# Kernel tuning notes

Hardware: AMD Instinct MI355X
Metric: run time of the kernel (lower is better)

Reference implementation:

```python
import jax, jax.numpy as jnp
import numpy as np

CHN = 64
C8 = CHN // 8          # 8
ANG_IN = 5
ANG_OUT = 5
BU, V, H, W = 8, ANG_IN, 64, 64


def setup_inputs() -> dict:
    key = jax.random.key(0)
    ks = jax.random.split(key, 7)
    s = 0.05
    buffer = jax.random.normal(ks[0], (BU, CHN, V, H, W), jnp.float32)
    # 1x1x1 Conv3d weights stored as [out_ch, in_ch]
    Wq = jax.random.normal(ks[1], (C8, CHN), jnp.float32) * s
    Wk = jax.random.normal(ks[2], (C8, CHN), jnp.float32) * s
    Wv = jax.random.normal(ks[3], (C8 * ANG_OUT, CHN), jnp.float32) * s
    Wc = jax.random.normal(ks[4], (C8 * ANG_OUT, CHN), jnp.float32) * s
    # out block: Conv3d(40->64, k=(1,1,7), pad (0,0,3)); Conv3d(64->64, k=(7,1,1), pad (3,0,0))
    W1 = jax.random.normal(ks[5], (CHN, C8 * ANG_IN, 1, 1, 7), jnp.float32) * s
    W2 = jax.random.normal(ks[6], (CHN, CHN, 7, 1, 1), jnp.float32) * s
    return {"buffer": buffer, "Wq": Wq, "Wk": Wk, "Wv": Wv, "Wc": Wc, "W1": W1, "W2": W2}


def _pointwise(Wo, x):
    # 1x1x1 Conv3d == channel GEMM
    return jnp.einsum('oc,bcvhw->bovhw', Wo, x)


def reference(buffer, Wq, Wk, Wv, Wc, W1, W2):
    bu, c, v, h, w = buffer.shape
    q = _pointwise(Wq, buffer)      # [bu, c8, v, h, w]
    k = _pointwise(Wk, buffer)      # [bu, c8, v, h, w]
    val = _pointwise(Wv, buffer)    # [bu, c8*ar_out, v, h, w]

    def flat(x):  # 'bu c v h w -> bu c h (v w)'
        return x.transpose(0, 1, 3, 2, 4).reshape(bu, x.shape[1], h, v * w)

    qf, kf, vf = flat(q), flat(k), flat(val)
    attn = jax.nn.softmax(jnp.einsum('bchm,bchn->bhmn', qf, kf), axis=-1)  # [bu,h,vw,vw]
    out = jnp.einsum('bhmn,bchn->bchm', attn, vf)                          # [bu,c8*ar_out,h,vw]
    out = out.reshape(bu, -1, h, v, w).transpose(0, 1, 3, 2, 4)            # [bu,c8*ar_out,v,h,w]

    out = out + _pointwise(Wc, buffer)
    # 'bu (c ar_out) v h w -> bu (c v) ar_out h w'
    c8 = out.shape[1] // ANG_OUT
    out = out.reshape(bu, c8, ANG_OUT, v, h, w).transpose(0, 1, 3, 2, 4, 5)
    out = out.reshape(bu, c8 * v, ANG_OUT, h, w)

    dn = ('NCDHW', 'OIDHW', 'NCDHW')
    out = jax.nn.relu(jax.lax.conv_general_dilated(
        out, W1, (1, 1, 1), [(0, 0), (0, 0), (3, 3)], dimension_numbers=dn))
    out = jax.nn.relu(jax.lax.conv_general_dilated(
        out, W2, (1, 1, 1), [(3, 3), (0, 0), (0, 0)], dimension_numbers=dn))
    return out  # [bu, chn, ar_out, h, w]
```

## Files before the change

kernel.cpp:

```cpp
#include <hip/hip_runtime.h>
#include <math.h>


typedef __attribute__((ext_vector_type(8))) short bf16x8;
typedef __attribute__((ext_vector_type(4))) short bf16x4;
typedef __attribute__((ext_vector_type(4))) float fp32x4;
typedef __attribute__((ext_vector_type(8))) unsigned short u16x8;

#define OFF_WP      0
#define OFF_Z       29696
#define OFF_W1P_US  12288
#define OFF_W2P_US  30720
#define OFF_QFH_US  13166592
#define OFF_KFH_US  14477312
#define OFF_VTH_US  15788032

__device__ inline unsigned short f2b(float f) {
    unsigned u = __builtin_bit_cast(unsigned, f);
    u = (u + 0x7fffu + ((u >> 16) & 1u)) >> 16;
    return (unsigned short)u;
}

#if __has_builtin(__builtin_amdgcn_mfma_f32_16x16x16bf16_1k)
#define MFMA16(a, b, c) __builtin_amdgcn_mfma_f32_16x16x16bf16_1k(a, b, c, 0, 0, 0)
#else
static __device__ inline fp32x4 mfma16_asm(bf16x4 a, bf16x4 b, fp32x4 c) {
    asm("v_mfma_f32_16x16x16_bf16 %0, %1, %2, %0" : "+v"(c) : "v"(a), "v"(b));
    return c;
}
#define MFMA16(a, b, c) mfma16_asm(a, b, c)
#endif

__global__ void prep_weights(const float* __restrict__ Wq, const float* __restrict__ Wk,
                             const float* __restrict__ Wv, const float* __restrict__ Wc,
                             const float* __restrict__ W1, const float* __restrict__ W2,
                             float* __restrict__ ws) {
    int e = blockIdx.x * 256 + threadIdx.x;
    unsigned short* us = (unsigned short*)ws;
    if (e < 6144) {
        int og = e / 1536, r = e % 1536;
        int c = r / 24, l = r % 24;
        int o = og * 24 + l;
        float v;
        if (o < 8)       v = Wq[o * 64 + c];
        else if (o < 16) v = Wk[(o - 8) * 64 + c];
        else if (o < 56) v = Wv[(o - 16) * 64 + c];
        else             v = Wc[(o - 56) * 64 + c];
        ws[OFF_WP + e] = v;
    } else if (e < 6144 + 18432) {
        int t = e - 6144;
        int j = t & 7, lane = (t >> 3) & 63, ks = (t >> 9) % 9, wid = t / 4608;
        int oc = wid * 16 + (lane & 15);
        int k = ks * 32 + (lane >> 4) * 8 + j;
        float v = 0.f;
        if (k < 280) { int kw = k / 40, ic = k % 40; v = W1[oc * 280 + ic * 7 + kw]; }
        us[OFF_W1P_US + t] = f2b(v);
    } else if (e < 6144 + 18432 + 28672) {
        int t = e - 6144 - 18432;
        int j = t & 7, lane = (t >> 3) & 63, kk = (t >> 9) & 1, kd = (t >> 10) % 7, wid = t / 7168;
        int oc = wid * 16 + (lane & 15);
        int ic = kk * 32 + (lane >> 4) * 8 + j;
        us[OFF_W2P_US + t] = f2b(W2[oc * 448 + ic * 7 + kd]);
    }
}

__global__ __launch_bounds__(256) void proj_kernel(const float* __restrict__ buf,
                                                   float* __restrict__ ws) {
    __shared__ alignas(16) float xs[64 * 64];
    int b = blockIdx.x;
    int h = b & 63;
    int v = (b >> 6) % 5;
    int bu = b / 320;
    int tid = threadIdx.x, wid = tid >> 6, w = tid & 63;

    const float* xbase = buf + ((bu * 64) * 5 + v) * 4096 + h * 64;
    for (int e = tid; e < 1024; e += 256) {
        int c = e >> 4, wq = e & 15;
        *(float4*)&xs[c * 64 + wq * 4] = *(const float4*)&xbase[c * 20480 + wq * 4];
    }
    __syncthreads();

    int og = __builtin_amdgcn_readfirstlane(wid);
    const float* wp = ws + OFF_WP + og * 1536;

    float acc[24];
    #pragma unroll
    for (int l = 0; l < 24; l++) acc[l] = 0.f;
    for (int c = 0; c < 64; c++) {
        float x = xs[c * 64 + w];
        const float* wr = wp + c * 24;
        #pragma unroll
        for (int l = 0; l < 24; l++) acc[l] += wr[l] * x;
    }

    int site = bu * 64 + h;
    int n = v * 64 + w;
    unsigned short* base = (unsigned short*)ws;
    unsigned short* qfh = base + OFF_QFH_US;
    unsigned short* kfh = base + OFF_KFH_US;
    unsigned short* vth = base + OFF_VTH_US;
    float* z = ws + OFF_Z;

    if (og == 0) {
        u16x8 qv, kv;
        #pragma unroll
        for (int l = 0; l < 8; l++) { qv[l] = f2b(acc[l]); kv[l] = f2b(acc[8 + l]); }
        *(u16x8*)&qfh[(site * 320 + n) * 8] = qv;
        *(u16x8*)&kfh[(site * 320 + n) * 8] = kv;
        #pragma unroll
        for (int l = 16; l < 24; l++) vth[(site * 48 + (l - 16)) * 320 + n] = f2b(acc[l]);
    } else if (og == 1) {
        #pragma unroll
        for (int l = 0; l < 24; l++) vth[(site * 48 + 8 + l) * 320 + n] = f2b(acc[l]);
    } else if (og == 2) {
        #pragma unroll
        for (int l = 0; l < 8; l++) vth[(site * 48 + 32 + l) * 320 + n] = f2b(acc[l]);
        #pragma unroll
        for (int l = 8; l < 24; l++) {
            int j2 = l - 8;
            int c8 = j2 / 5, ar = j2 % 5;
            z[((bu * 40 + c8 * 5 + v) * 5 + ar) * 4096 + h * 64 + w] = acc[l];
        }
    } else {
        #pragma unroll
        for (int l = 0; l < 24; l++) {
            int j2 = 16 + l;
            int c8 = j2 / 5, ar = j2 % 5;
            z[((bu * 40 + c8 * 5 + v) * 5 + ar) * 4096 + h * 64 + w] = acc[l];
        }
        #pragma unroll
        for (int j = 40; j < 48; j++)
            vth[(site * 48 + j) * 320 + n] = (j == 40) ? (unsigned short)0x3F80 : (unsigned short)0;
    }
}

__global__ __launch_bounds__(256, 2) void attn_kernel(float* __restrict__ ws) {
    __shared__ alignas(16) short vt[48 * 328];

    int bid = blockIdx.x;
    int chunk = bid >> 9;
    int site = bid & 511;
    int bu = site >> 6, h = site & 63;
    int tid = threadIdx.x;
    int wid = tid >> 6, lane = tid & 63;
    int col = lane & 15, quad = lane >> 4;

    const unsigned short* base = (const unsigned short*)ws;
    const unsigned short* qfh = base + OFF_QFH_US + site * 320 * 8;
    const unsigned short* kfh = base + OFF_KFH_US + site * 320 * 8;
    const unsigned short* vsrc = base + OFF_VTH_US + site * 48 * 320;
    float* z = ws + OFF_Z;

    for (int e = tid; e < 48 * 40; e += 256) {
        int row = e / 40, c8o = e % 40;
        *(u16x8*)&vt[row * 328 + c8o * 8] = *(const u16x8*)&vsrc[row * 320 + c8o * 8];
    }
    __syncthreads();

    int off0[4], off1[4], off2[4];
    #pragma unroll
    for (int r = 0; r < 4; r++) {
        int j0 = quad * 4 + r, j1 = j0 + 16, j2 = j0 + 32;
        off0[r] = ((j0 / 5) * 25 + j0 % 5) * 4096;
        off1[r] = ((j1 / 5) * 25 + j1 % 5) * 4096;
        off2[r] = ((j2 / 5) * 25 + j2 % 5) * 4096;
    }

    int mt = chunk * 4 + wid;
    int m0 = mt * 16;

    bf16x8 qa = (bf16x8)0;
    if (quad == 0) qa = *(const bf16x8*)&qfh[(m0 + col) * 8];

    fp32x4 acc0 = {0.f, 0.f, 0.f, 0.f}, acc1 = acc0, acc2 = acc0;

    for (int cc = 0; cc < 4; cc++) {
        fp32x4 sT[5];
        #pragma unroll
        for (int u = 0; u < 5; u++) {
            int nt = cc * 5 + u;
            bf16x8 kb = (bf16x8)0;
            if (quad == 0) kb = *(const bf16x8*)&kfh[(nt * 16 + col) * 8];
            sT[u] = __builtin_amdgcn_mfma_f32_16x16x32_bf16(
                kb, qa, (fp32x4){0.f, 0.f, 0.f, 0.f}, 0, 0, 0);
        }
        #pragma unroll
        for (int u = 0; u < 5; u++) {
            int nt = cc * 5 + u;
            bf16x4 pa;
            #pragma unroll
            for (int r = 0; r < 4; r++) pa[r] = (short)f2b(__expf(sT[u][r]));
            const short* vb = &vt[nt * 16 + quad * 4];
            acc0 = MFMA16(*(const bf16x4*)&vb[(col) * 328],      pa, acc0);
            acc1 = MFMA16(*(const bf16x4*)&vb[(16 + col) * 328], pa, acc1);
            acc2 = MFMA16(*(const bf16x4*)&vb[(32 + col) * 328], pa, acc2);
        }
    }

    float L = __shfl(acc2[0], 32 + col, 64);
    float inv = 1.f / L;

    int v_idx = m0 >> 6, w0 = m0 & 63;
    float* zb = z + (bu * 200 + v_idx * 5) * 4096 + h * 64 + w0 + col;
    #pragma unroll
    for (int r = 0; r < 4; r++) {
        zb[off0[r]] += acc0[r] * inv;
        zb[off1[r]] += acc1[r] * inv;
        if (quad < 2) zb[off2[r]] += acc2[r] * inv;
    }
}

__global__ __launch_bounds__(256) void conv12_mfma(float* __restrict__ ws,
                                                   float* __restrict__ out) {
    __shared__ alignas(16) unsigned short ol[320 * 72];
    __shared__ alignas(16) unsigned short zl2[2][72 * 40];
    int b = blockIdx.x;
    int bu = b >> 6, h = b & 63;
    int tid = threadIdx.x, wid = tid >> 6, lane = tid & 63;
    int col = lane & 15, quad = lane >> 4;
    const float* z = ws + OFF_Z;

    const unsigned short* w1p = (const unsigned short*)ws + OFF_W1P_US;
    bf16x8 a1[9];
    #pragma unroll
    for (int ks = 0; ks < 9; ks++)
        a1[ks] = *(const bf16x8*)&w1p[((wid * 9 + ks) * 64 + lane) * 8];

    #define STAGE_AR(ar_, bufi_)                                                          \
        {                                                                                 \
            unsigned short* zb_ = zl2[bufi_];                                             \
            if (tid < 160) {                                                              \
                int wpi = tid / 20, icd = tid % 20;                                       \
                int wp = wpi < 3 ? wpi : wpi + 64;                                        \
                ((unsigned*)zb_)[wp * 20 + icd] = 0u;                                     \
            }                                                                             \
            for (int icq = wid; icq < 10; icq += 4) {                                     \
                const float* src = z + ((bu * 40 + icq * 4) * 5 + (ar_)) * 4096 + h * 64 + lane; \
                ushort4 v4;                                                               \
                v4.x = f2b(src[0]);                                                       \
                v4.y = f2b(src[5 * 4096]);                                                \
                v4.z = f2b(src[10 * 4096]);                                               \
                v4.w = f2b(src[15 * 4096]);                                               \
                *(ushort4*)&zb_[(3 + lane) * 40 + icq * 4] = v4;                          \
            }                                                                             \
        }

    STAGE_AR(0, 0);
    __syncthreads();
    for (int ar = 0; ar < 5; ar++) {
        if (ar < 4) STAGE_AR(ar + 1, (ar + 1) & 1);
        const unsigned short* zb = zl2[ar & 1];
        #pragma unroll
        for (int w4 = 0; w4 < 4; w4++) {
            int bb = (w4 * 16 + col) * 40;
            fp32x4 acc = {0.f, 0.f, 0.f, 0.f};
            #pragma unroll
            for (int ks = 0; ks < 9; ks++) {
                bf16x8 bf = *(const bf16x8*)&zb[bb + ks * 32 + quad * 8];
                acc = __builtin_amdgcn_mfma_f32_16x16x32_bf16(a1[ks], bf, acc, 0, 0, 0);
            }
            ushort4 o;
            o.x = f2b(fmaxf(acc[0], 0.f));
            o.y = f2b(fmaxf(acc[1], 0.f));
            o.z = f2b(fmaxf(acc[2], 0.f));
            o.w = f2b(fmaxf(acc[3], 0.f));
            *(ushort4*)&ol[(ar * 64 + w4 * 16 + col) * 72 + wid * 16 + quad * 4] = o;
        }
        __syncthreads();
    }
    #undef STAGE_AR

    const unsigned short* w2p = (const unsigned short*)ws + OFF_W2P_US;
    bf16x8 a2[7][2];
    #pragma unroll
    for (int kd = 0; kd < 7; kd++)
        #pragma unroll
        for (int kk = 0; kk < 2; kk++)
            a2[kd][kk] = *(const bf16x8*)&w2p[(((wid * 7 + kd) * 2 + kk) * 64 + lane) * 8];

    for (int nt = 0; nt < 20; nt++) {
        int ar = nt >> 2, wbase = (nt & 3) * 16;
        fp32x4 acc = {0.f, 0.f, 0.f, 0.f};
        #pragma unroll
        for (int kd = 0; kd < 7; kd++) {
            int arp = ar + kd - 3;
            if (arp >= 0 && arp < 5) {
                int sb = (arp * 64 + wbase + col) * 72;
                #pragma unroll
                for (int kk = 0; kk < 2; kk++) {
                    bf16x8 bf = *(const bf16x8*)&ol[sb + kk * 32 + quad * 8];
                    acc = __builtin_amdgcn_mfma_f32_16x16x32_bf16(a2[kd][kk], bf, acc, 0, 0, 0);
                }
            }
        }
        int w = wbase + col;
        #pragma unroll
        for (int r = 0; r < 4; r++) {
            int oc = wid * 16 + quad * 4 + r;
            out[((bu * 64 + oc) * 5 + ar) * 4096 + h * 64 + w] = fmaxf(acc[r], 0.f);
        }
    }
}

extern "C" void kernel_launch(void* const* d_in, const int* in_sizes, int n_in,
                              void* d_out, int out_size, void* d_ws, size_t ws_size,
                              hipStream_t stream) {
    const float* buf = (const float*)d_in[0];
    const float* Wq  = (const float*)d_in[1];
    const float* Wk  = (const float*)d_in[2];
    const float* Wv  = (const float*)d_in[3];
    const float* Wc  = (const float*)d_in[4];
    const float* W1  = (const float*)d_in[5];
    const float* W2  = (const float*)d_in[6];
    float* ws  = (float*)d_ws;
    float* out = (float*)d_out;

    prep_weights<<<208, 256, 0, stream>>>(Wq, Wk, Wv, Wc, W1, W2, ws);
    proj_kernel<<<2560, 256, 0, stream>>>(buf, ws);
    attn_kernel<<<2560, 256, 0, stream>>>(ws);
    conv12_mfma<<<512, 256, 0, stream>>>(ws, out);
}
```

Baseline: 171.3 us.

## Split conv kernel along width into halves and pack projection FMAs

The conv12 kernel now gives each block half of the width (32 columns plus a 3-column halo on each side), doubling the grid from 512 to 1024 blocks and halving shared memory per block. This raises occupancy and parallelism on the many-CU device. The cost is redundant staging of the halo columns and one more block launch per site. Separately, the projection kernel's inner loop accumulates in float2 vectors so the compiler can emit packed FMA instructions.

```diff
diff --git a/kernel.cpp b/kernel.cpp
--- a/kernel.cpp
+++ b/kernel.cpp
@@ -5,6 +5,7 @@
 typedef __attribute__((ext_vector_type(8))) short bf16x8;
 typedef __attribute__((ext_vector_type(4))) short bf16x4;
 typedef __attribute__((ext_vector_type(4))) float fp32x4;
+typedef __attribute__((ext_vector_type(2))) float fp32x2;
 typedef __attribute__((ext_vector_type(8))) unsigned short u16x8;
 
 #define OFF_WP      0
@@ -83,15 +84,19 @@
     int og = __builtin_amdgcn_readfirstlane(wid);
     const float* wp = ws + OFF_WP + og * 1536;
 
-    float acc[24];
-    #pragma unroll
-    for (int l = 0; l < 24; l++) acc[l] = 0.f;
+    fp32x2 acc2[12];
+    #pragma unroll
+    for (int l = 0; l < 12; l++) acc2[l] = (fp32x2){0.f, 0.f};
     for (int c = 0; c < 64; c++) {
         float x = xs[c * 64 + w];
-        const float* wr = wp + c * 24;
-        #pragma unroll
-        for (int l = 0; l < 24; l++) acc[l] += wr[l] * x;
-    }
+        fp32x2 xv = {x, x};
+        const fp32x2* wr2 = (const fp32x2*)(wp + c * 24);
+        #pragma unroll
+        for (int l = 0; l < 12; l++) acc2[l] += wr2[l] * xv;
+    }
+    float acc[24];
+    #pragma unroll
+    for (int l = 0; l < 12; l++) { acc[2 * l] = acc2[l][0]; acc[2 * l + 1] = acc2[l][1]; }
 
     int site = bu * 64 + h;
     int n = v * 64 + w;
@@ -212,10 +217,13 @@
 
 __global__ __launch_bounds__(256) void conv12_mfma(float* __restrict__ ws,
                                                    float* __restrict__ out) {
-    __shared__ alignas(16) unsigned short ol[320 * 72];
-    __shared__ alignas(16) unsigned short zl2[2][72 * 40];
+    __shared__ alignas(16) unsigned short ol[160 * 72];
+    __shared__ alignas(16) unsigned short zl2[2][38 * 40];
     int b = blockIdx.x;
-    int bu = b >> 6, h = b & 63;
+    int wh = b >> 9;
+    int site = b & 511;
+    int bu = site >> 6, h = site & 63;
+    int whbase = wh * 32;
     int tid = threadIdx.x, wid = tid >> 6, lane = tid & 63;
     int col = lane & 15, quad = lane >> 4;
     const float* z = ws + OFF_Z;
@@ -226,22 +234,21 @@
     for (int ks = 0; ks < 9; ks++)
         a1[ks] = *(const bf16x8*)&w1p[((wid * 9 + ks) * 64 + lane) * 8];
 
+    int wprime = whbase - 3 + lane;
+    bool wvalid = (lane < 38) && (wprime >= 0) && (wprime < 64);
     #define STAGE_AR(ar_, bufi_)                                                          \
         {                                                                                 \
             unsigned short* zb_ = zl2[bufi_];                                             \
-            if (tid < 160) {                                                              \
-                int wpi = tid / 20, icd = tid % 20;                                       \
-                int wp = wpi < 3 ? wpi : wpi + 64;                                        \
-                ((unsigned*)zb_)[wp * 20 + icd] = 0u;                                     \
-            }                                                                             \
             for (int icq = wid; icq < 10; icq += 4) {                                     \
-                const float* src = z + ((bu * 40 + icq * 4) * 5 + (ar_)) * 4096 + h * 64 + lane; \
-                ushort4 v4;                                                               \
-                v4.x = f2b(src[0]);                                                       \
-                v4.y = f2b(src[5 * 4096]);                                                \
-                v4.z = f2b(src[10 * 4096]);                                               \
-                v4.w = f2b(src[15 * 4096]);                                               \
-                *(ushort4*)&zb_[(3 + lane) * 40 + icq * 4] = v4;                          \
+                ushort4 v4 = {0, 0, 0, 0};                                                \
+                if (wvalid) {                                                             \
+                    const float* src = z + ((bu * 40 + icq * 4) * 5 + (ar_)) * 4096 + h * 64 + wprime; \
+                    v4.x = f2b(src[0]);                                                   \
+                    v4.y = f2b(src[5 * 4096]);                                            \
+                    v4.z = f2b(src[10 * 4096]);                                           \
+                    v4.w = f2b(src[15 * 4096]);                                           \
+                }                                                                         \
+                if (lane < 38) *(ushort4*)&zb_[lane * 40 + icq * 4] = v4;                 \
             }                                                                             \
         }
 
@@ -251,7 +258,7 @@
         if (ar < 4) STAGE_AR(ar + 1, (ar + 1) & 1);
         const unsigned short* zb = zl2[ar & 1];
         #pragma unroll
-        for (int w4 = 0; w4 < 4; w4++) {
+        for (int w4 = 0; w4 < 2; w4++) {
             int bb = (w4 * 16 + col) * 40;
             fp32x4 acc = {0.f, 0.f, 0.f, 0.f};
             #pragma unroll
@@ -264,7 +271,7 @@
             o.y = f2b(fmaxf(acc[1], 0.f));
             o.z = f2b(fmaxf(acc[2], 0.f));
             o.w = f2b(fmaxf(acc[3], 0.f));
-            *(ushort4*)&ol[(ar * 64 + w4 * 16 + col) * 72 + wid * 16 + quad * 4] = o;
+            *(ushort4*)&ol[(ar * 32 + w4 * 16 + col) * 72 + wid * 16 + quad * 4] = o;
         }
         __syncthreads();
     }
@@ -278,14 +285,14 @@
         for (int kk = 0; kk < 2; kk++)
             a2[kd][kk] = *(const bf16x8*)&w2p[(((wid * 7 + kd) * 2 + kk) * 64 + lane) * 8];
 
-    for (int nt = 0; nt < 20; nt++) {
-        int ar = nt >> 2, wbase = (nt & 3) * 16;
+    for (int nt = 0; nt < 10; nt++) {
+        int ar = nt >> 1, wbase = (nt & 1) * 16;
         fp32x4 acc = {0.f, 0.f, 0.f, 0.f};
         #pragma unroll
         for (int kd = 0; kd < 7; kd++) {
             int arp = ar + kd - 3;
             if (arp >= 0 && arp < 5) {
-                int sb = (arp * 64 + wbase + col) * 72;
+                int sb = (arp * 32 + wbase + col) * 72;
                 #pragma unroll
                 for (int kk = 0; kk < 2; kk++) {
                     bf16x8 bf = *(const bf16x8*)&ol[sb + kk * 32 + quad * 8];
@@ -293,7 +300,7 @@
                 }
             }
         }
-        int w = wbase + col;
+        int w = whbase + wbase + col;
         #pragma unroll
         for (int r = 0; r < 4; r++) {
             int oc = wid * 16 + quad * 4 + r;
@@ -318,5 +325,5 @@
     prep_weights<<<208, 256, 0, stream>>>(Wq, Wk, Wv, Wc, W1, W2, ws);
     proj_kernel<<<2560, 256, 0, stream>>>(buf, ws);
     attn_kernel<<<2560, 256, 0, stream>>>(ws);
-    conv12_mfma<<<512, 256, 0, stream>>>(ws, out);
-}
+    conv12_mfma<<<1024, 256, 0, stream>>>(ws, out);
+}
```

Result: slower. 177.3 us (+3.5%).
